# Optimization experiments

Measured on AMD Instinct MI355X. Metric: run time of the kernel, lower is better.

Reference implementation:

```python
import jax, jax.numpy as jnp
import numpy as np

B, S, D, H = 4, 2048, 1024, 16  # batch, seq, d_hidden, n_heads


def setup_inputs() -> dict:
    key = jax.random.key(0)
    ks = jax.random.split(key, 7)
    scale = 1.0 / np.sqrt(D)
    return {
        "x": jax.random.normal(ks[0], (B, S, D), dtype=jnp.float32),
        "Wq": jax.random.normal(ks[1], (D, D), dtype=jnp.float32) * scale,
        "bq": jax.random.normal(ks[2], (D,), dtype=jnp.float32) * 0.02,
        "Wk": jax.random.normal(ks[3], (D, D), dtype=jnp.float32) * scale,
        "bk": jax.random.normal(ks[4], (D,), dtype=jnp.float32) * 0.02,
        "Wv": jax.random.normal(ks[5], (D, D), dtype=jnp.float32) * scale,
        "bv": jax.random.normal(ks[6], (D,), dtype=jnp.float32) * 0.02,
    }


def reference(x, Wq, bq, Wk, bk, Wv, bv):
    n_heads = H
    head_dim = D // n_heads

    def proj(inp, W, b):
        # torch nn.Linear: y = x @ W^T + b
        y = jnp.einsum("bsd,ed->bse", inp, W) + b
        # split last dim into (H, Wd) then transpose to (B, H, S, Wd)
        return y.reshape(inp.shape[0], inp.shape[1], n_heads, head_dim).transpose(0, 2, 1, 3)

    q = proj(x, Wq, bq)
    k = proj(x, Wk, bk)
    v = proj(x, Wv, bv)

    # scores: (B, H, S, S)
    scores = jnp.einsum("bhqd,bhkd->bhqk", q, k) / jnp.sqrt(jnp.asarray(head_dim, q.dtype))
    attn = jax.nn.softmax(scores, axis=-1)
    h = jnp.einsum("bhqk,bhkd->bhqd", attn, v)  # (B, H, S, Wd)
    h = h.transpose(0, 2, 1, 3).reshape(x.shape[0], x.shape[1], D)  # merge heads
    return h
```

## Files before the change

kernel.cpp:

```cpp
#include <hip/hip_runtime.h>
#include <hip/hip_bf16.h>

#define B_ 4
#define S_ 2048
#define D_ 1024
#define H_ 16
#define HD 64

typedef __bf16 bf16;
typedef __bf16 bf16x4 __attribute__((ext_vector_type(4)));
typedef __bf16 bf16x8 __attribute__((ext_vector_type(8)));
typedef float f32x4 __attribute__((ext_vector_type(4)));
typedef float f32x16 __attribute__((ext_vector_type(16)));

#define LOG2E 1.4426950408889634f

__device__ inline void gload_lds16(const bf16* g, bf16* l) {
    __builtin_amdgcn_global_load_lds(
        (const __attribute__((address_space(1))) void*)g,
        (__attribute__((address_space(3))) void*)l, 16, 0, 0);
}

__device__ inline int swz(int row, int colb) {
    return row * 64 + ((colb ^ ((row & 7) << 4)) >> 1);
}

__device__ inline unsigned cvt_pk_bf16(float lo, float hi) {
    unsigned r;
    asm("v_cvt_pk_bf16_f32 %0, %1, %2" : "=v"(r) : "v"(lo), "v"(hi));
    return r;
}

__global__ void cast_pack_kernel(const float* __restrict__ x,
                                 const float* __restrict__ Wq,
                                 const float* __restrict__ Wk,
                                 const float* __restrict__ Wv,
                                 bf16* __restrict__ Xb, bf16* __restrict__ Wb) {
    const long XN = (long)B_ * S_ * D_;
    const long WN = (long)D_ * D_;
    long i4 = ((long)blockIdx.x * blockDim.x + threadIdx.x) * 4;
    if (i4 < XN) {
        float4 v = *(const float4*)(x + i4);
        bf16* o = Xb + i4;
        o[0] = (bf16)v.x; o[1] = (bf16)v.y; o[2] = (bf16)v.z; o[3] = (bf16)v.w;
    } else {
        long j = i4 - XN;
        if (j < 3 * WN) {
            int which = (int)(j / WN);
            long jj = j - (long)which * WN;
            const float* src = which == 0 ? Wq : which == 1 ? Wk : Wv;
            float4 v = *(const float4*)(src + jj);
            bf16* o = Wb + j;
            o[0] = (bf16)v.x; o[1] = (bf16)v.y; o[2] = (bf16)v.z; o[3] = (bf16)v.w;
        }
    }
}

#define GM 128
#define GN 128
#define GK 64

__global__ __launch_bounds__(256) void gemm_qkv_kernel(
    const bf16* __restrict__ Xb, const bf16* __restrict__ Wb,
    const float* __restrict__ bq, const float* __restrict__ bk,
    const float* __restrict__ bv,
    bf16* __restrict__ Qg, bf16* __restrict__ Kg, bf16* __restrict__ Vt) {
    __shared__ bf16 SMEM[GM * GK + GN * GK];
    bf16* As = SMEM;
    bf16* Bs = SMEM + GM * GK;
    const int tid = threadIdx.x;
    const int lane = tid & 63;
    const int wid = tid >> 6;
    const int col = lane & 15, grp = lane >> 4;

    const int id = blockIdx.x;
    const int id2 = (id & 7) * 192 + (id >> 3);
    const int m0 = (id2 / 24) * GM;
    const int n0 = (id2 % 24) * GN;
    const int wr = wid >> 1, wc = wid & 1;

    const f32x4 zf = {0.f, 0.f, 0.f, 0.f};
    f32x4 acc[4][4];
#pragma unroll
    for (int m = 0; m < 4; m++)
#pragma unroll
        for (int n = 0; n < 4; n++) acc[m][n] = zf;

    for (int kt = 0; kt < D_ / GK; ++kt) {
        const int k0 = kt * GK;
#pragma unroll
        for (int i = 0; i < 4; i++) {
            int fl = i * 2048 + wid * 512 + lane * 8;
            int r = fl >> 6, c = fl & 63;
            gload_lds16(Xb + (size_t)(m0 + r) * D_ + k0 + c, As + i * 2048 + wid * 512);
        }
#pragma unroll
        for (int i = 0; i < 4; i++) {
            int fl = i * 2048 + wid * 512 + lane * 8;
            int r = fl >> 6, c = fl & 63;
            gload_lds16(Wb + (size_t)(n0 + r) * D_ + k0 + c, Bs + i * 2048 + wid * 512);
        }
        __syncthreads();
#pragma unroll
        for (int kk = 0; kk < 2; ++kk) {
            bf16x8 a[4], b[4];
#pragma unroll
            for (int m = 0; m < 4; m++)
                a[m] = *(const bf16x8*)(As + (wr * 64 + m * 16 + col) * GK + kk * 32 + grp * 8);
#pragma unroll
            for (int n = 0; n < 4; n++)
                b[n] = *(const bf16x8*)(Bs + (wc * 64 + n * 16 + col) * GK + kk * 32 + grp * 8);
#pragma unroll
            for (int m = 0; m < 4; m++)
#pragma unroll
                for (int n = 0; n < 4; n++)
                    acc[m][n] = __builtin_amdgcn_mfma_f32_16x16x32_bf16(a[m], b[n], acc[m][n], 0, 0, 0);
        }
        __syncthreads();
    }

    const int which = n0 >> 10;
    if (which == 2) {
        bf16* Vl = SMEM;
#pragma unroll
        for (int n = 0; n < 4; n++) {
            int dl = wc * 64 + n * 16 + col;
            float bias = bv[(n0 - 2048) + dl];
#pragma unroll
            for (int m = 0; m < 4; m++) {
                bf16x4 pv;
#pragma unroll
                for (int i = 0; i < 4; i++) pv[i] = (bf16)(acc[m][n][i] + bias);
                int sl = wr * 64 + m * 16 + grp * 4;
                *(bf16x4*)(&Vl[dl * 128 + (sl ^ ((dl & 7) << 3))]) = pv;
            }
        }
        __syncthreads();
#pragma unroll
        for (int c0 = 0; c0 < 8; c0++) {
            int c = c0 * 256 + tid;
            int dl = c >> 4, s8 = (c & 15) * 8;
            bf16x8 val = *(const bf16x8*)(&Vl[dl * 128 + (s8 ^ ((dl & 7) << 3))]);
            int s = m0 + s8;
            int b = s >> 11, sl = s & 2047;
            int dglob = (n0 - 2048) + dl;
            int h = dglob >> 6, dd = dglob & 63;
            *(bf16x8*)(&Vt[((size_t)(b * H_ + h) * HD + dd) * S_ + sl]) = val;
        }
    } else {
        const float* bp = which == 0 ? bq : bk;
        bf16* dst = which == 0 ? Qg : Kg;
        const float qsc = which == 0 ? (0.125f * LOG2E) : 1.0f;
#pragma unroll
        for (int n = 0; n < 4; n++) {
            int e = n0 + wc * 64 + n * 16 + col;
            int ee = e & 1023;
            float bias = bp[ee];
            int h = ee >> 6, d = ee & 63;
#pragma unroll
            for (int m = 0; m < 4; m++) {
#pragma unroll
                for (int i = 0; i < 4; i++) {
                    int s = m0 + wr * 64 + m * 16 + grp * 4 + i;
                    int b = s >> 11, sl = s & 2047;
                    dst[((size_t)(b * H_ + h) * S_ + sl) * HD + d] =
                        (bf16)((acc[m][n][i] + bias) * qsc);
                }
            }
        }
    }
}

#define KB 64

__global__ __launch_bounds__(512, 4) void attn_kernel(
    const bf16* __restrict__ Qg, const bf16* __restrict__ Kg,
    const bf16* __restrict__ Vt, float* __restrict__ out) {
    __shared__ bf16 Ks[2][64 * 64];
    __shared__ bf16 Vs[2][64 * 64];
    const int tid = threadIdx.x, lane = tid & 63, wid = tid >> 6;
    const int l31 = lane & 31, hi = lane >> 5;

    const int id = blockIdx.x;
    const int swzid = (id & 7) * 64 + (id >> 3);
    const int bh = swzid >> 3;
    const int q0 = (swzid & 7) * 256 + wid * 32;

    const bf16* Kbase = Kg + (size_t)bh * S_ * HD;
    const bf16* Vbase = Vt + (size_t)bh * HD * S_;

    const int r0 = tid >> 3;
    const int cb = ((tid & 7) * 16) ^ ((r0 & 7) << 4);
    const bf16* ksrc = Kbase + (size_t)r0 * HD + (cb >> 1);
    const bf16* vsrc = Vbase + (size_t)r0 * S_ + (cb >> 1);

#define STAGE(bsel, kv0)                                            \
    do {                                                            \
        gload_lds16(ksrc + (size_t)(kv0)*HD, &Ks[bsel][wid * 512]); \
        gload_lds16(vsrc + (kv0), &Vs[bsel][wid * 512]);            \
    } while (0)

    bf16x8 qa[4];
#pragma unroll
    for (int ks = 0; ks < 4; ks++)
        qa[ks] = *(const bf16x8*)(Qg + ((size_t)bh * S_ + q0 + l31) * HD + ks * 16 + hi * 8);

    const f32x16 z16 = {0.f, 0.f, 0.f, 0.f, 0.f, 0.f, 0.f, 0.f,
                        0.f, 0.f, 0.f, 0.f, 0.f, 0.f, 0.f, 0.f};
    f32x16 o[2];
    o[0] = z16; o[1] = z16;
    f32x4 ls = {0.f, 0.f, 0.f, 0.f};

    int cur = 0;
    STAGE(0, 0);
    __syncthreads();

    for (int t = 0; t < S_ / KB; ++t) {
        if (t < S_ / KB - 1) STAGE(cur ^ 1, (t + 1) * KB);

        f32x16 sc[2];
        __builtin_amdgcn_s_setprio(1);
#pragma unroll
        for (int kvt = 0; kvt < 2; kvt++) {
            {
                bf16x8 kb = *(const bf16x8*)(&Ks[cur][swz(kvt * 32 + l31, hi * 16)]);
                sc[kvt] = __builtin_amdgcn_mfma_f32_32x32x16_bf16(kb, qa[0], z16, 0, 0, 0);
            }
#pragma unroll
            for (int ks = 1; ks < 4; ks++) {
                bf16x8 kb = *(const bf16x8*)(&Ks[cur][swz(kvt * 32 + l31, ks * 32 + hi * 16)]);
                sc[kvt] = __builtin_amdgcn_mfma_f32_32x32x16_bf16(kb, qa[ks], sc[kvt], 0, 0, 0);
            }
        }
        __builtin_amdgcn_s_setprio(0);

        bf16x8 pa[4];
#pragma unroll
        for (int kvt = 0; kvt < 2; kvt++) {
            float p[16];
#pragma unroll
            for (int r = 0; r < 16; r++) p[r] = __builtin_amdgcn_exp2f(sc[kvt][r]);
            f32x4 s0 = {p[0], p[1], p[2], p[3]};
            f32x4 s1 = {p[4], p[5], p[6], p[7]};
            f32x4 s2 = {p[8], p[9], p[10], p[11]};
            f32x4 s3 = {p[12], p[13], p[14], p[15]};
            ls += (s0 + s1) + (s2 + s3);
#pragma unroll
            for (int b = 0; b < 2; b++) {
                unsigned A  = cvt_pk_bf16(p[8 * b + 0], p[8 * b + 1]);
                unsigned Bw = cvt_pk_bf16(p[8 * b + 4], p[8 * b + 5]);
                unsigned C  = cvt_pk_bf16(p[8 * b + 2], p[8 * b + 3]);
                unsigned Dw = cvt_pk_bf16(p[8 * b + 6], p[8 * b + 7]);
                asm("v_permlane32_swap_b32 %0, %1" : "+v"(A), "+v"(Bw));
                asm("v_permlane32_swap_b32 %0, %1" : "+v"(C), "+v"(Dw));
                union { unsigned u[4]; bf16x8 v; } pk;
                pk.u[0] = A; pk.u[1] = C; pk.u[2] = Bw; pk.u[3] = Dw;
                pa[kvt * 2 + b] = pk.v;
            }
        }

        __builtin_amdgcn_s_setprio(1);
#pragma unroll
        for (int ks2 = 0; ks2 < 4; ks2++) {
#pragma unroll
            for (int dt = 0; dt < 2; dt++) {
                bf16x8 vb = *(const bf16x8*)(&Vs[cur][swz(dt * 32 + l31, ks2 * 32 + hi * 16)]);
                o[dt] = __builtin_amdgcn_mfma_f32_32x32x16_bf16(vb, pa[ks2], o[dt], 0, 0, 0);
            }
        }
        __builtin_amdgcn_s_setprio(0);

        __syncthreads();
        cur ^= 1;
    }

    float denom = ls[0] + ls[1] + ls[2] + ls[3];
    denom += __shfl_xor(denom, 32);
    float inv = 1.f / denom;

    int b = bh >> 4, h = bh & 15;
    int q = q0 + l31;
    float* obase = out + ((size_t)(b * S_ + q)) * D_ + h * HD;
#pragma unroll
    for (int dt = 0; dt < 2; dt++)
#pragma unroll
        for (int g = 0; g < 4; g++) {
            f32x4 r = {o[dt][4 * g + 0] * inv, o[dt][4 * g + 1] * inv,
                       o[dt][4 * g + 2] * inv, o[dt][4 * g + 3] * inv};
            *(f32x4*)(obase + dt * 32 + 8 * g + 4 * hi) = r;
        }
#undef STAGE
}

extern "C" void kernel_launch(void* const* d_in, const int* in_sizes, int n_in,
                              void* d_out, int out_size, void* d_ws, size_t ws_size,
                              hipStream_t stream) {
    const float* x  = (const float*)d_in[0];
    const float* Wq = (const float*)d_in[1];
    const float* bq = (const float*)d_in[2];
    const float* Wk = (const float*)d_in[3];
    const float* bk = (const float*)d_in[4];
    const float* Wv = (const float*)d_in[5];
    const float* bv = (const float*)d_in[6];
    float* out = (float*)d_out;

    bf16* ws = (bf16*)d_ws;
    bf16* Xb = ws;
    bf16* Wb = Xb + (size_t)B_ * S_ * D_;
    bf16* Qg = Wb + (size_t)3 * D_ * D_;
    bf16* Kg = Qg + (size_t)B_ * S_ * D_;
    bf16* Vt = Kg + (size_t)B_ * S_ * D_;

    hipLaunchKernelGGL(cast_pack_kernel,
                       dim3((B_ * S_ * D_ + 3 * D_ * D_) / (4 * 256)), dim3(256), 0, stream,
                       x, Wq, Wk, Wv, Xb, Wb);
    hipLaunchKernelGGL(gemm_qkv_kernel, dim3(24 * 64), dim3(256), 0, stream,
                       Xb, Wb, bq, bk, bv, Qg, Kg, Vt);
    hipLaunchKernelGGL(attn_kernel, dim3(512), dim3(512), 0, stream,
                       Qg, Kg, Vt, out);
}
```

Before: 176.1 us.

## Double-buffer QKV GEMM with larger 128x256 tiles and swizzled LDS

```diff
diff --git a/kernel.cpp b/kernel.cpp
--- a/kernel.cpp
+++ b/kernel.cpp
@@ -56,28 +56,38 @@
     }
 }
 
-#define GM 128
-#define GN 128
-#define GK 64
-
-__global__ __launch_bounds__(256) void gemm_qkv_kernel(
+#define TM 128
+#define TN 256
+#define TK 64
+
+__global__ __launch_bounds__(512, 2) void gemm_qkv_kernel(
     const bf16* __restrict__ Xb, const bf16* __restrict__ Wb,
     const float* __restrict__ bq, const float* __restrict__ bk,
     const float* __restrict__ bv,
     bf16* __restrict__ Qg, bf16* __restrict__ Kg, bf16* __restrict__ Vt) {
-    __shared__ bf16 SMEM[GM * GK + GN * GK];
+    __shared__ bf16 SMEM[49152];
     bf16* As = SMEM;
-    bf16* Bs = SMEM + GM * GK;
+    bf16* Bs = SMEM + 16384;
     const int tid = threadIdx.x;
     const int lane = tid & 63;
     const int wid = tid >> 6;
     const int col = lane & 15, grp = lane >> 4;
+    const int wr = wid >> 2, wc = wid & 3;
 
     const int id = blockIdx.x;
-    const int id2 = (id & 7) * 192 + (id >> 3);
-    const int m0 = (id2 / 24) * GM;
-    const int n0 = (id2 % 24) * GN;
-    const int wr = wid >> 1, wc = wid & 1;
+    const int id2 = (id & 7) * 96 + (id >> 3);
+    const int m0 = (id2 / 12) * TM;
+    const int n0 = (id2 % 12) * TN;
+
+    const int r8 = tid >> 3;
+    const int cbs = ((tid & 7) * 16) ^ ((r8 & 7) << 4);
+    const bf16* asrc = Xb + (size_t)(m0 + r8) * D_ + (cbs >> 1);
+    const bf16* bsrc = Wb + (size_t)(n0 + r8) * D_ + (cbs >> 1);
+
+#define STAGE_A(c, kt, j) \
+    gload_lds16(asrc + (size_t)(j) * 64 * D_ + (kt) * TK, As + (c) * 8192 + (j) * 4096 + wid * 512)
+#define STAGE_B(c, kt, j) \
+    gload_lds16(bsrc + (size_t)(j) * 64 * D_ + (kt) * TK, Bs + (c) * 16384 + (j) * 4096 + wid * 512)
 
     const f32x4 zf = {0.f, 0.f, 0.f, 0.f};
     f32x4 acc[4][4];
@@ -86,41 +96,72 @@
 #pragma unroll
         for (int n = 0; n < 4; n++) acc[m][n] = zf;
 
-    for (int kt = 0; kt < D_ / GK; ++kt) {
-        const int k0 = kt * GK;
-#pragma unroll
-        for (int i = 0; i < 4; i++) {
-            int fl = i * 2048 + wid * 512 + lane * 8;
-            int r = fl >> 6, c = fl & 63;
-            gload_lds16(Xb + (size_t)(m0 + r) * D_ + k0 + c, As + i * 2048 + wid * 512);
-        }
-#pragma unroll
-        for (int i = 0; i < 4; i++) {
-            int fl = i * 2048 + wid * 512 + lane * 8;
-            int r = fl >> 6, c = fl & 63;
-            gload_lds16(Wb + (size_t)(n0 + r) * D_ + k0 + c, Bs + i * 2048 + wid * 512);
-        }
-        __syncthreads();
-#pragma unroll
-        for (int kk = 0; kk < 2; ++kk) {
+    STAGE_A(0, 0, 0); STAGE_A(0, 0, 1);
+    STAGE_B(0, 0, 0); STAGE_B(0, 0, 1); STAGE_B(0, 0, 2); STAGE_B(0, 0, 3);
+    asm volatile("s_waitcnt vmcnt(0)");
+    __builtin_amdgcn_s_barrier();
+
+    int c = 0;
+#pragma unroll 1
+    for (int kt = 0; kt < D_ / TK; ++kt) {
+        const bf16* Ac = As + c * 8192;
+        const bf16* Bc = Bs + c * 16384;
+        {
             bf16x8 a[4], b[4];
 #pragma unroll
             for (int m = 0; m < 4; m++)
-                a[m] = *(const bf16x8*)(As + (wr * 64 + m * 16 + col) * GK + kk * 32 + grp * 8);
+                a[m] = *(const bf16x8*)(Ac + swz(wr * 64 + m * 16 + col, grp * 16));
 #pragma unroll
             for (int n = 0; n < 4; n++)
-                b[n] = *(const bf16x8*)(Bs + (wc * 64 + n * 16 + col) * GK + kk * 32 + grp * 8);
+                b[n] = *(const bf16x8*)(Bc + swz(wc * 64 + n * 16 + col, grp * 16));
+            if (kt < D_ / TK - 1) {
+                STAGE_A(c ^ 1, kt + 1, 0); STAGE_A(c ^ 1, kt + 1, 1);
+                STAGE_B(c ^ 1, kt + 1, 0);
+            }
+            __builtin_amdgcn_s_barrier();
+            asm volatile("s_waitcnt lgkmcnt(0)");
+            __builtin_amdgcn_sched_barrier(0);
+            __builtin_amdgcn_s_setprio(1);
 #pragma unroll
             for (int m = 0; m < 4; m++)
 #pragma unroll
                 for (int n = 0; n < 4; n++)
                     acc[m][n] = __builtin_amdgcn_mfma_f32_16x16x32_bf16(a[m], b[n], acc[m][n], 0, 0, 0);
-        }
-        __syncthreads();
+            __builtin_amdgcn_s_setprio(0);
+            __builtin_amdgcn_s_barrier();
+        }
+        {
+            bf16x8 a[4], b[4];
+#pragma unroll
+            for (int m = 0; m < 4; m++)
+                a[m] = *(const bf16x8*)(Ac + swz(wr * 64 + m * 16 + col, 64 + grp * 16));
+#pragma unroll
+            for (int n = 0; n < 4; n++)
+                b[n] = *(const bf16x8*)(Bc + swz(wc * 64 + n * 16 + col, 64 + grp * 16));
+            if (kt < D_ / TK - 1) {
+                STAGE_B(c ^ 1, kt + 1, 1); STAGE_B(c ^ 1, kt + 1, 2); STAGE_B(c ^ 1, kt + 1, 3);
+            }
+            __builtin_amdgcn_s_barrier();
+            asm volatile("s_waitcnt lgkmcnt(0)");
+            __builtin_amdgcn_sched_barrier(0);
+            __builtin_amdgcn_s_setprio(1);
+#pragma unroll
+            for (int m = 0; m < 4; m++)
+#pragma unroll
+                for (int n = 0; n < 4; n++)
+                    acc[m][n] = __builtin_amdgcn_mfma_f32_16x16x32_bf16(a[m], b[n], acc[m][n], 0, 0, 0);
+            __builtin_amdgcn_s_setprio(0);
+            asm volatile("s_waitcnt vmcnt(0)");
+            __builtin_amdgcn_s_barrier();
+        }
+        c ^= 1;
     }
+#undef STAGE_A
+#undef STAGE_B
 
     const int which = n0 >> 10;
     if (which == 2) {
+        __syncthreads();
         bf16* Vl = SMEM;
 #pragma unroll
         for (int n = 0; n < 4; n++) {
@@ -138,8 +179,8 @@
         __syncthreads();
 #pragma unroll
         for (int c0 = 0; c0 < 8; c0++) {
-            int c = c0 * 256 + tid;
-            int dl = c >> 4, s8 = (c & 15) * 8;
+            int cc = c0 * 512 + tid;
+            int dl = cc >> 4, s8 = (cc & 15) * 8;
             bf16x8 val = *(const bf16x8*)(&Vl[dl * 128 + (s8 ^ ((dl & 7) << 3))]);
             int s = m0 + s8;
             int b = s >> 11, sl = s & 2047;
@@ -314,7 +355,7 @@
     hipLaunchKernelGGL(cast_pack_kernel,
                        dim3((B_ * S_ * D_ + 3 * D_ * D_) / (4 * 256)), dim3(256), 0, stream,
                        x, Wq, Wk, Wv, Xb, Wb);
-    hipLaunchKernelGGL(gemm_qkv_kernel, dim3(24 * 64), dim3(256), 0, stream,
+    hipLaunchKernelGGL(gemm_qkv_kernel, dim3(64 * 12), dim3(512), 0, stream,
                        Xb, Wb, bq, bk, bv, Qg, Kg, Vt);
     hipLaunchKernelGGL(attn_kernel, dim3(512), dim3(512), 0, stream,
                        Qg, Kg, Vt, out);
```

New measurement: 159.4 us. -9.5%, faster.
